# Performance work log

Hardware: AMD Instinct MI355X
Metric: run time of the kernel (lower is better)

The kernel has to match this reference:

```python
import jax, jax.numpy as jnp
import numpy as np

FEAT_DIM, M, K, D = 1024, 32, 256, 32
B = 8192
ALPHA = 1.0
BN_EPS = 1e-5
NORM_EPS = 1e-12  # F.normalize eps


def _l2_normalize(v, axis=-1):
    # matches torch F.normalize: v / max(||v||, eps)
    n = jnp.sqrt(jnp.sum(v * v, axis=axis, keepdims=True))
    return v / jnp.maximum(n, NORM_EPS)


def setup_inputs() -> dict:
    key = jax.random.key(0)
    kx, kc = jax.random.split(key)
    x = jax.random.normal(kx, (B, FEAT_DIM), dtype=jnp.float32)
    # xavier-uniform init over (M,K,D) then per-codeword L2 normalization (as in __init__)
    limit = float(np.sqrt(6.0 / (K + D)))
    C_k = jax.random.uniform(kc, (M, K, D), dtype=jnp.float32, minval=-limit, maxval=limit)
    C_k = _l2_normalize(C_k, axis=-1)
    return {"x": x, "C_k": C_k}


def reference(x, C_k):
    Bn = x.shape[0]
    x_ = x.reshape(Bn, M, D)                       # (B, M, D)
    x_norm_ = _l2_normalize(x_, axis=-1)           # per-subspace normalize
    x_normalized = x_norm_.reshape(Bn, FEAT_DIM)

    # per-subspace similarity: (B, M, K)
    sims = jnp.einsum('bmd,mkd->bmk', x_norm_, C_k)

    # BatchNorm1d(M, affine=False) in training mode: normalize per channel m over (B, K)
    mean = jnp.mean(sims, axis=(0, 2), keepdims=True)
    var = jnp.mean(jnp.square(sims - mean), axis=(0, 2), keepdims=True)  # biased var
    sims = (sims - mean) / jnp.sqrt(var + BN_EPS)

    # hard assignment + codeword gather (C_v == C_k in VQ mode)
    hard_codes = jnp.argmax(sims, axis=-1)                     # (B, M) int
    x_hat_hard_ = C_k[jnp.arange(M)[None, :], hard_codes]      # (B, M, D)
    x_hat_hard = x_hat_hard_.reshape(Bn, FEAT_DIM)

    # soft assignment (mask_topK is None)
    soft_codes = jax.nn.softmax(sims * ALPHA, axis=-1)         # (B, M, K)

    # straight-through: value = x_hat_hard, grad flows through x_normalized
    x_hat = x_normalized - jax.lax.stop_gradient(x_normalized - x_hat_hard)

    # pq_detach_opt == 'features'
    reg_loss = jnp.sum(jnp.square(jax.lax.stop_gradient(x_normalized) - x_hat_hard), axis=-1)  # (B,)

    return (x_hat, hard_codes, soft_codes, x_normalized, reg_loss)
```

## Files before the change

kernel.cpp:

```cpp
#include <hip/hip_runtime.h>
#include <cmath>

#define FEAT_DIM 1024
#define MM 32
#define KK 256
#define DD 32
#define BB 8192

constexpr float BN_EPS = 1e-5f;

typedef float f32x4 __attribute__((ext_vector_type(4)));

__device__ __forceinline__ float wave_fsum(float v) {
    #pragma unroll
    for (int s = 32; s >= 1; s >>= 1) v += __shfl_xor(v, s);
    return v;
}

template <int CTRL, int RM = 0xf>
__device__ __forceinline__ float dppf(float v) {
    int r = __builtin_amdgcn_update_dpp(__builtin_bit_cast(int, v),
                                        __builtin_bit_cast(int, v),
                                        CTRL, RM, 0xf, false);
    return __builtin_bit_cast(float, r);
}
__device__ __forceinline__ float wave_dpp_max(float v) {
    v = fmaxf(v, dppf<0xB1>(v));
    v = fmaxf(v, dppf<0x4E>(v));
    v = fmaxf(v, dppf<0x141>(v));
    v = fmaxf(v, dppf<0x140>(v));
    v = fmaxf(v, dppf<0x142, 0xa>(v));
    v = fmaxf(v, dppf<0x143, 0xc>(v));
    return __builtin_bit_cast(float, __builtin_amdgcn_readlane(__builtin_bit_cast(int, v), 63));
}
__device__ __forceinline__ float wave_dpp_sum(float v) {
    v += dppf<0xB1>(v);
    v += dppf<0x4E>(v);
    v += dppf<0x141>(v);
    v += dppf<0x140>(v);
    v += dppf<0x142, 0xa>(v);
    v += dppf<0x143, 0xc>(v);
    return __builtin_bit_cast(float, __builtin_amdgcn_readlane(__builtin_bit_cast(int, v), 63));
}

__global__ void k_norm(const float* __restrict__ x, float* __restrict__ xn,
                       double* __restrict__ stats) {
    if (blockIdx.x == 0 && threadIdx.x < 2 * MM) stats[threadIdx.x] = 0.0;
    const int t = blockIdx.x * blockDim.x + threadIdx.x;
    float4 v = ((const float4*)x)[t];
    float ss = v.x*v.x + v.y*v.y + v.z*v.z + v.w*v.w;
    #pragma unroll
    for (int s = 1; s < 8; s <<= 1) ss += __shfl_xor(ss, s);
    const float r = 1.0f / fmaxf(sqrtf(ss), 1e-12f);
    float4 o = {v.x*r, v.y*r, v.z*r, v.w*r};
    ((float4*)xn)[t] = o;
}

__global__ void k_gram(const float* __restrict__ Ck, float* __restrict__ G,
                       float* __restrict__ S) {
    __shared__ float CT[DD][KK + 4];
    const int m = blockIdx.x, part = blockIdx.y;
    const int t = threadIdx.x, wid = t >> 6, lane = t & 63;
    const float4* cp = (const float4*)(Ck + ((size_t)m * KK + t) * DD);
    #pragma unroll
    for (int i = 0; i < 8; ++i) {
        float4 v = cp[i];
        CT[4*i+0][t] = v.x; CT[4*i+1][t] = v.y;
        CT[4*i+2][t] = v.z; CT[4*i+3][t] = v.w;
    }
    __syncthreads();
    #pragma unroll 1
    for (int ei = 0; ei < 32; ++ei) {
        const int e = part * 128 + wid * 32 + ei;
        const int i = e >> 5, j = e & 31;
        float acc = 0.f;
        #pragma unroll
        for (int c4 = 0; c4 < 4; ++c4)
            acc = fmaf(CT[i][lane + 64*c4], CT[j][lane + 64*c4], acc);
        acc = wave_fsum(acc);
        if (lane == 0) G[((size_t)m * DD + i) * DD + j] = acc;
    }
    if (part == 0 && wid == 0) {
        #pragma unroll 1
        for (int d = 0; d < DD; ++d) {
            float a = 0.f;
            #pragma unroll
            for (int c4 = 0; c4 < 4; ++c4) a += CT[d][lane + 64*c4];
            a = wave_fsum(a);
            if (lane == 0) S[m * DD + d] = a;
        }
    }
}

__global__ void k_stats2(const float* __restrict__ xn, const float* __restrict__ G,
                         const float* __restrict__ S, double* __restrict__ stats) {
    const int m = blockIdx.x;
    const int b = blockIdx.y * 256 + threadIdx.x;
    float xv[DD];
    {
        const float4* xp = (const float4*)(xn + (size_t)b * FEAT_DIM + m * DD);
        #pragma unroll
        for (int i = 0; i < 8; ++i) {
            float4 v = xp[i];
            xv[4*i+0]=v.x; xv[4*i+1]=v.y; xv[4*i+2]=v.z; xv[4*i+3]=v.w;
        }
    }
    const float4* Gp = (const float4*)(G + (size_t)m * DD * DD);
    const float*  Sp = S + m * DD;
    float q = 0.f, s = 0.f;
    #pragma unroll 4
    for (int i = 0; i < DD; ++i) {
        float y = 0.f;
        #pragma unroll
        for (int jv = 0; jv < 8; ++jv) {
            float4 g = Gp[i * 8 + jv];
            y = fmaf(g.x, xv[4*jv+0], y); y = fmaf(g.y, xv[4*jv+1], y);
            y = fmaf(g.z, xv[4*jv+2], y); y = fmaf(g.w, xv[4*jv+3], y);
        }
        q = fmaf(y, xv[i], q);
    }
    #pragma unroll
    for (int i = 0; i < DD; ++i) s = fmaf(Sp[i], xv[i], s);
    q = wave_fsum(q); s = wave_fsum(s);
    __shared__ float lq[4], ls[4];
    const int wid = threadIdx.x >> 6, lane = threadIdx.x & 63;
    if (lane == 0) { lq[wid] = q; ls[wid] = s; }
    __syncthreads();
    if (threadIdx.x == 0) {
        atomicAdd(&stats[2*m],   (double)((ls[0]+ls[1])+(ls[2]+ls[3])));
        atomicAdd(&stats[2*m+1], (double)((lq[0]+lq[1])+(lq[2]+lq[3])));
    }
}

template <int BT>
__global__ __launch_bounds__(256, 2)
void k_main(const float* __restrict__ xn, const float* __restrict__ Ck,
            const double* __restrict__ stats,
            float* __restrict__ xhat, float* __restrict__ hard,
            float* __restrict__ soft, float* __restrict__ part) {
    const int m = blockIdx.x;
    const int wid = threadIdx.x >> 6, lane = threadIdx.x & 63;

    const double Ninv = 1.0 / ((double)BB * (double)KK);
    const double mu  = stats[2*m] * Ninv;
    const double var = stats[2*m+1] * Ninv - mu * mu;
    const float rstd = (float)(1.0 / sqrt(var + (double)BN_EPS));

    float c[4][DD];
    #pragma unroll
    for (int j = 0; j < 4; ++j) {
        const float4* cp = (const float4*)(Ck + ((size_t)m * KK + 4*lane + j) * DD);
        #pragma unroll
        for (int i = 0; i < 8; ++i) {
            float4 v = cp[i];
            c[j][4*i+0]=v.x; c[j][4*i+1]=v.y; c[j][4*i+2]=v.z; c[j][4*i+3]=v.w;
        }
    }

    const int b_base = blockIdx.y * (4 * BT) + wid;

    auto loadslice = [&](float4 (&q)[8], int b) {
        const int bu = __builtin_amdgcn_readfirstlane(b);
        const float4* xp = (const float4*)(xn + (size_t)bu * FEAT_DIM + m * DD);
        #pragma unroll
        for (int i = 0; i < 8; ++i) q[i] = xp[i];
    };

    auto process = [&](const float4 (&q)[8], int b) {
        float d0=0.f, d1=0.f, d2=0.f, d3=0.f;
        #pragma unroll
        for (int i = 0; i < 8; ++i) {
            const float4 q4 = q[i];
            d0 = fmaf(q4.x, c[0][4*i+0], d0); d0 = fmaf(q4.y, c[0][4*i+1], d0);
            d0 = fmaf(q4.z, c[0][4*i+2], d0); d0 = fmaf(q4.w, c[0][4*i+3], d0);
            d1 = fmaf(q4.x, c[1][4*i+0], d1); d1 = fmaf(q4.y, c[1][4*i+1], d1);
            d1 = fmaf(q4.z, c[1][4*i+2], d1); d1 = fmaf(q4.w, c[1][4*i+3], d1);
            d2 = fmaf(q4.x, c[2][4*i+0], d2); d2 = fmaf(q4.y, c[2][4*i+1], d2);
            d2 = fmaf(q4.z, c[2][4*i+2], d2); d2 = fmaf(q4.w, c[2][4*i+3], d2);
            d3 = fmaf(q4.x, c[3][4*i+0], d3); d3 = fmaf(q4.y, c[3][4*i+1], d3);
            d3 = fmaf(q4.z, c[3][4*i+2], d3); d3 = fmaf(q4.w, c[3][4*i+3], d3);
        }

        const float p0 = __expf((d0 - 1.f) * rstd);
        const float p1 = __expf((d1 - 1.f) * rstd);
        const float p2 = __expf((d2 - 1.f) * rstd);
        const float p3 = __expf((d3 - 1.f) * rstd);

        const float mx = wave_dpp_max(fmaxf(fmaxf(d0, d1), fmaxf(d2, d3)));
        const unsigned long long m0 = __ballot(d0 == mx);
        const unsigned long long m1 = __ballot(d1 == mx);
        const unsigned long long m2 = __ballot(d2 == mx);
        const unsigned long long m3 = __ballot(d3 == mx);
        const int k0 = m0 ? 4*__builtin_ctzll(m0)+0 : 0x7fffffff;
        const int k1 = m1 ? 4*__builtin_ctzll(m1)+1 : 0x7fffffff;
        const int k2 = m2 ? 4*__builtin_ctzll(m2)+2 : 0x7fffffff;
        const int k3 = m3 ? 4*__builtin_ctzll(m3)+3 : 0x7fffffff;
        const int bi = min(min(k0, k1), min(k2, k3));

        const float tot = wave_dpp_sum((p0 + p1) + (p2 + p3));
        const float inv = 1.0f / tot;

        f32x4 o = {p0*inv, p1*inv, p2*inv, p3*inv};
        __builtin_nontemporal_store(o, (f32x4*)(soft + ((size_t)b * MM + m) * KK) + lane);
        if (lane == 0) {
            hard[(size_t)b * MM + m] = (float)bi;
            part[(size_t)m * BB + b] = 2.f - 2.f * mx;
        }
        if (lane < 8) {
            f32x4 cw = ((const f32x4*)(Ck + ((size_t)m * KK + bi) * DD))[lane];
            __builtin_nontemporal_store(cw, (f32x4*)(xhat + (size_t)b * FEAT_DIM + m * DD) + lane);
        }
    };

    float4 A[8], Bv[8];
    loadslice(A, b_base);
    #pragma unroll 1
    for (int it = 0; it < BT; it += 2) {
        loadslice(Bv, b_base + 4 * (it + 1));
        process(A, b_base + 4 * it);
        if (it + 2 < BT) loadslice(A, b_base + 4 * (it + 2));
        process(Bv, b_base + 4 * (it + 1));
    }
}

__global__ void k_regsum(const float* __restrict__ part, float* __restrict__ reg) {
    const int b = blockIdx.x * 256 + threadIdx.x;
    float a = 0.f;
    #pragma unroll
    for (int mm = 0; mm < MM; ++mm) a += part[(size_t)mm * BB + b];
    reg[b] = a;
}

extern "C" void kernel_launch(void* const* d_in, const int* in_sizes, int n_in,
                              void* d_out, int out_size, void* d_ws, size_t ws_size,
                              hipStream_t stream) {
    const float* x  = (const float*)d_in[0];
    const float* Ck = (const float*)d_in[1];

    float* out   = (float*)d_out;
    float* xhat  = out;
    float* hard  = xhat  + (size_t)BB * FEAT_DIM;
    float* soft  = hard  + (size_t)BB * MM;
    float* xnorm = soft  + (size_t)BB * MM * KK;
    float* reg   = xnorm + (size_t)BB * FEAT_DIM;

    double* stats = (double*)d_ws;
    float* partb  = (float*)d_ws + 256;
    float* Gbuf = soft;
    float* Sbuf = soft + (size_t)MM * DD * DD;

    k_norm<<<(BB * FEAT_DIM / 4) / 256, 256, 0, stream>>>(x, xnorm, stats);
    k_gram<<<dim3(MM, 8), 256, 0, stream>>>(Ck, Gbuf, Sbuf);
    k_stats2<<<dim3(MM, BB / 256), 256, 0, stream>>>(xnorm, Gbuf, Sbuf, stats);
    constexpr int BT = 32;
    k_main<BT><<<dim3(MM, BB / (4 * BT)), 256, 0, stream>>>(xnorm, Ck, stats, xhat, hard, soft, partb);
    k_regsum<<<BB / 256, 256, 0, stream>>>(partb, reg);
}
```

Before: 168.0 us.

## Software-pipeline dot products ahead of softmax finish and use exp2/rcp

Splits the per-row work into a dot-product stage and a finish stage (softmax, argmax, stores), then interleaves them so the dot for the next row overlaps the reductions and stores of the current one. Loads are prefetched two rows ahead, with the row index clamped to stay in bounds. The exponent now uses exp2 with a folded log2e scale and drops the constant shift of 1, and the reciprocal uses the hardware rcp. Removing the shift relies on dot products being bounded, since both vectors are unit-normalized, so exp cannot overflow. The extra live registers may hurt occupancy.

```diff
diff --git a/kernel.cpp b/kernel.cpp
--- a/kernel.cpp
+++ b/kernel.cpp
@@ -145,6 +145,7 @@
     const double mu  = stats[2*m] * Ninv;
     const double var = stats[2*m+1] * Ninv - mu * mu;
     const float rstd = (float)(1.0 / sqrt(var + (double)BN_EPS));
+    const float c1 = rstd * 1.4426950408889634f;
 
     float c[4][DD];
     #pragma unroll
@@ -160,37 +161,41 @@
     const int b_base = blockIdx.y * (4 * BT) + wid;
 
     auto loadslice = [&](float4 (&q)[8], int b) {
-        const int bu = __builtin_amdgcn_readfirstlane(b);
+        int bu = __builtin_amdgcn_readfirstlane(b);
+        bu = min(bu, BB - 1);
         const float4* xp = (const float4*)(xn + (size_t)bu * FEAT_DIM + m * DD);
         #pragma unroll
         for (int i = 0; i < 8; ++i) q[i] = xp[i];
     };
 
-    auto process = [&](const float4 (&q)[8], int b) {
-        float d0=0.f, d1=0.f, d2=0.f, d3=0.f;
+    auto DOT = [&](const float4 (&q)[8], float (&dd)[4]) {
+        float a0=0.f, a1=0.f, a2=0.f, a3=0.f;
         #pragma unroll
         for (int i = 0; i < 8; ++i) {
             const float4 q4 = q[i];
-            d0 = fmaf(q4.x, c[0][4*i+0], d0); d0 = fmaf(q4.y, c[0][4*i+1], d0);
-            d0 = fmaf(q4.z, c[0][4*i+2], d0); d0 = fmaf(q4.w, c[0][4*i+3], d0);
-            d1 = fmaf(q4.x, c[1][4*i+0], d1); d1 = fmaf(q4.y, c[1][4*i+1], d1);
-            d1 = fmaf(q4.z, c[1][4*i+2], d1); d1 = fmaf(q4.w, c[1][4*i+3], d1);
-            d2 = fmaf(q4.x, c[2][4*i+0], d2); d2 = fmaf(q4.y, c[2][4*i+1], d2);
-            d2 = fmaf(q4.z, c[2][4*i+2], d2); d2 = fmaf(q4.w, c[2][4*i+3], d2);
-            d3 = fmaf(q4.x, c[3][4*i+0], d3); d3 = fmaf(q4.y, c[3][4*i+1], d3);
-            d3 = fmaf(q4.z, c[3][4*i+2], d3); d3 = fmaf(q4.w, c[3][4*i+3], d3);
-        }
-
-        const float p0 = __expf((d0 - 1.f) * rstd);
-        const float p1 = __expf((d1 - 1.f) * rstd);
-        const float p2 = __expf((d2 - 1.f) * rstd);
-        const float p3 = __expf((d3 - 1.f) * rstd);
-
-        const float mx = wave_dpp_max(fmaxf(fmaxf(d0, d1), fmaxf(d2, d3)));
-        const unsigned long long m0 = __ballot(d0 == mx);
-        const unsigned long long m1 = __ballot(d1 == mx);
-        const unsigned long long m2 = __ballot(d2 == mx);
-        const unsigned long long m3 = __ballot(d3 == mx);
+            a0 = fmaf(q4.x, c[0][4*i+0], a0); a0 = fmaf(q4.y, c[0][4*i+1], a0);
+            a0 = fmaf(q4.z, c[0][4*i+2], a0); a0 = fmaf(q4.w, c[0][4*i+3], a0);
+            a1 = fmaf(q4.x, c[1][4*i+0], a1); a1 = fmaf(q4.y, c[1][4*i+1], a1);
+            a1 = fmaf(q4.z, c[1][4*i+2], a1); a1 = fmaf(q4.w, c[1][4*i+3], a1);
+            a2 = fmaf(q4.x, c[2][4*i+0], a2); a2 = fmaf(q4.y, c[2][4*i+1], a2);
+            a2 = fmaf(q4.z, c[2][4*i+2], a2); a2 = fmaf(q4.w, c[2][4*i+3], a2);
+            a3 = fmaf(q4.x, c[3][4*i+0], a3); a3 = fmaf(q4.y, c[3][4*i+1], a3);
+            a3 = fmaf(q4.z, c[3][4*i+2], a3); a3 = fmaf(q4.w, c[3][4*i+3], a3);
+        }
+        dd[0]=a0; dd[1]=a1; dd[2]=a2; dd[3]=a3;
+    };
+
+    auto FINISH = [&](const float (&dd)[4], int b) {
+        const float p0 = exp2f(dd[0] * c1);
+        const float p1 = exp2f(dd[1] * c1);
+        const float p2 = exp2f(dd[2] * c1);
+        const float p3 = exp2f(dd[3] * c1);
+
+        const float mx = wave_dpp_max(fmaxf(fmaxf(dd[0], dd[1]), fmaxf(dd[2], dd[3])));
+        const unsigned long long m0 = __ballot(dd[0] == mx);
+        const unsigned long long m1 = __ballot(dd[1] == mx);
+        const unsigned long long m2 = __ballot(dd[2] == mx);
+        const unsigned long long m3 = __ballot(dd[3] == mx);
         const int k0 = m0 ? 4*__builtin_ctzll(m0)+0 : 0x7fffffff;
         const int k1 = m1 ? 4*__builtin_ctzll(m1)+1 : 0x7fffffff;
         const int k2 = m2 ? 4*__builtin_ctzll(m2)+2 : 0x7fffffff;
@@ -198,7 +203,7 @@
         const int bi = min(min(k0, k1), min(k2, k3));
 
         const float tot = wave_dpp_sum((p0 + p1) + (p2 + p3));
-        const float inv = 1.0f / tot;
+        const float inv = __builtin_amdgcn_rcpf(tot);
 
         f32x4 o = {p0*inv, p1*inv, p2*inv, p3*inv};
         __builtin_nontemporal_store(o, (f32x4*)(soft + ((size_t)b * MM + m) * KK) + lane);
@@ -212,14 +217,19 @@
         }
     };
 
-    float4 A[8], Bv[8];
-    loadslice(A, b_base);
+    float4 XA[8], XB[8];
+    float dA[4], dB[4];
+    loadslice(XA, b_base);
+    DOT(XA, dA);
+    loadslice(XB, b_base + 4);
     #pragma unroll 1
     for (int it = 0; it < BT; it += 2) {
-        loadslice(Bv, b_base + 4 * (it + 1));
-        process(A, b_base + 4 * it);
-        if (it + 2 < BT) loadslice(A, b_base + 4 * (it + 2));
-        process(Bv, b_base + 4 * (it + 1));
+        loadslice(XA, b_base + 4 * (it + 2));
+        DOT(XB, dB);
+        FINISH(dA, b_base + 4 * it);
+        loadslice(XB, b_base + 4 * (it + 3));
+        DOT(XA, dA);
+        FINISH(dB, b_base + 4 * (it + 1));
     }
 }
 
```

Result: slower. 361.5 us (+115.2%).
